# Optimization experiments

Measured on AMD Instinct MI355X. Metric: run time of the kernel, lower is better.

The kernel has to match this reference:

```python
import jax, jax.numpy as jnp
import numpy as np

HEADS = 8
DIM = 64      # dim
DH = 64       # dim_head
DK = 24       # dim_k (== dim_head_k * heads, required by reshape in forward)
DHK = 3       # dim_head_k (also conv groups)


def setup_inputs() -> dict:
    key = jax.random.key(0)
    ks = jax.random.split(key, 10)
    b, h, w = 4, 128, 128
    return {
        "x_in": jax.random.normal(ks[0], (b, h, w, DIM), jnp.float32),
        "illu_fea_trans": jax.random.normal(ks[1], (b, h, w, DIM), jnp.float32),
        "illu_map_trans": jax.random.normal(ks[2], (b, h, w, DK), jnp.float32),
        # Linear weights stored as [in, out] (torch stores [out, in]; math y = x @ W_in_out)
        "Wq": jax.random.normal(ks[3], (DIM, HEADS * DH), jnp.float32) * 0.05,
        "Wk": jax.random.normal(ks[4], (DK, HEADS * DHK), jnp.float32) * 0.05,
        "Wv": jax.random.normal(ks[5], (DIM, HEADS * DH), jnp.float32) * 0.05,
        "rescale": jnp.ones((HEADS, 1, 1), jnp.float32),
        "Wp": jax.random.normal(ks[6], (HEADS * DHK, DK), jnp.float32) * 0.05,
        "bp": jax.random.normal(ks[7], (DK,), jnp.float32) * 0.05,
        # grouped conv weights, OIHW: [out=24, in/groups=8, 3, 3]
        "conv1_w": jax.random.normal(ks[8], (DK, DK // DHK, 3, 3), jnp.float32) * 0.05,
        "conv2_w": jax.random.normal(ks[9], (DK, DK // DHK, 3, 3), jnp.float32) * 0.05,
    }


def _gconv(x_nchw, w_oihw):
    return jax.lax.conv_general_dilated(
        x_nchw, w_oihw, window_strides=(1, 1), padding='SAME',
        feature_group_count=DHK,
        dimension_numbers=('NCHW', 'OIHW', 'NCHW'))


def reference(x_in, illu_fea_trans, illu_map_trans, Wq, Wk, Wv, rescale, Wp, bp, conv1_w, conv2_w):
    b, h, w, c = x_in.shape
    n = h * w
    # projections
    q = (x_in.reshape(b, n, c) @ Wq).reshape(b, n, HEADS, DH)
    k_inp = illu_map_trans.reshape(b, n, DK) @ Wk            # [b, n, heads*dhk]
    v = (illu_fea_trans.reshape(b, n, c) @ Wv).reshape(b, n, HEADS, DH)
    kh = k_inp.reshape(b, n, HEADS, DHK)
    q = q / (DIM ** 0.5)  # note: scaled by sqrt(dim), not sqrt(dim_head)
    # channel-wise cross-attention: attn over channel dims, contracting tokens n
    attn = jnp.einsum('bnhk,bnhd->bhkd', kh, q) * rescale[None]  # [b, heads, dhk, dh]
    attn = jax.nn.softmax(attn, axis=-1)
    out = jnp.einsum('bhkd,bnhd->bnkh', attn, v)             # [b, n, dhk, heads]
    out = out.reshape(b, n, DHK * HEADS) @ Wp + bp           # proj
    out = out.reshape(b, h, w, DK)
    # positional branch: two grouped 3x3 convs with exact GELU on k_inp
    kx = k_inp.reshape(b, h, w, DK).transpose(0, 3, 1, 2)    # NCHW
    y = _gconv(kx, conv1_w)
    y = jax.nn.gelu(y, approximate=False)
    y = _gconv(y, conv2_w)
    return out + y.transpose(0, 2, 3, 1)
```

## Files before the change

kernel.cpp:

```cpp
#include <hip/hip_runtime.h>
#include <math.h>

#define HEADS 8
#define DIM   64
#define DK    24
#define DHK   3
#define BB    4
#define HH    128
#define WW    128
#define NN    (HH*WW)
#define QSCALE 0.125f

__global__ __launch_bounds__(1024) void s_reduce(
    const float* __restrict__ imap,
    const float* __restrict__ x,
    float* __restrict__ Sp_part,
    float* __restrict__ Pt)
{
    __shared__ float part[16 * 1540];
    const int tid = threadIdx.x;
    const int blk = blockIdx.x;
    const int b = blk >> 6, chunk = blk & 63;
    const int w = tid >> 6, lane = tid & 63;
    const int cq = lane & 15;
    const int ig = lane >> 4;

    const long tok0 = (long)b * NN + chunk * 256 + w * 16;
    const float* xp = x    + tok0 * 64 + cq * 4;
    const float* mp = imap + tok0 * 24 + ig * 6;

    float acc[6][4];
    #pragma unroll
    for (int r = 0; r < 6; ++r)
        #pragma unroll
        for (int q = 0; q < 4; ++q) acc[r][q] = 0.f;

    #pragma unroll 4
    for (int t = 0; t < 16; ++t) {
        float4 xv = *(const float4*)(xp + t * 64);
        float2 m0 = *(const float2*)(mp + t * 24);
        float2 m1 = *(const float2*)(mp + t * 24 + 2);
        float2 m2 = *(const float2*)(mp + t * 24 + 4);
        float mm[6] = {m0.x, m0.y, m1.x, m1.y, m2.x, m2.y};
        #pragma unroll
        for (int r = 0; r < 6; ++r) {
            acc[r][0] += mm[r] * xv.x;
            acc[r][1] += mm[r] * xv.y;
            acc[r][2] += mm[r] * xv.z;
            acc[r][3] += mm[r] * xv.w;
        }
    }

    float* pp = part + w * 1540;
    #pragma unroll
    for (int r = 0; r < 6; ++r) {
        float4 v = {acc[r][0], acc[r][1], acc[r][2], acc[r][3]};
        *(float4*)(pp + (ig * 6 + r) * 64 + cq * 4) = v;
    }
    __syncthreads();

    for (int e = tid; e < 1536; e += 1024) {
        float s = 0.f;
        #pragma unroll
        for (int ww = 0; ww < 16; ++ww) s += part[ww * 1540 + e];
        Sp_part[(long)blk * 1536 + e] = s;
    }
    if (blk < 4)
        for (int e = tid; e < 1536; e += 1024) Pt[blk * 1536 + e] = 0.f;
}

__global__ __launch_bounds__(256) void attn_fused(
    const float* __restrict__ Sp_part,
    const float* __restrict__ Wk,
    const float* __restrict__ Wq,
    const float* __restrict__ Wv,
    const float* __restrict__ rescale,
    const float* __restrict__ Wp,
    float* __restrict__ Pt)
{
    __shared__ float Sp_l[1536];
    __shared__ float sS[192];
    __shared__ float sP[192];
    __shared__ float Wv_l[64 * 65];

    const int tid = threadIdx.x, blk = blockIdx.x;
    const int b = blk >> 3, h = blk & 7;
    const int w = tid >> 6, lane = tid & 63;

    {
        float s[6] = {0.f, 0.f, 0.f, 0.f, 0.f, 0.f};
        const float* p = Sp_part + (long)(b * 64) * 1536 + tid;
        #pragma unroll 8
        for (int pb = 0; pb < 64; ++pb)
            #pragma unroll
            for (int k = 0; k < 6; ++k)
                s[k] += p[(long)pb * 1536 + k * 256];
        #pragma unroll
        for (int k = 0; k < 6; ++k) Sp_l[tid + k * 256] = s[k];
    }
    for (int e = tid; e < 4096; e += 256) {
        int c = e >> 6, d = e & 63;
        Wv_l[c * 65 + d] = Wv[c * 512 + h * 64 + d];
    }
    __syncthreads();

    if (w < 3) {
        const float* wk = Wk + (h * 3 + w);
        float s = 0.f;
        #pragma unroll
        for (int i = 0; i < 24; ++i) s += wk[i * 24] * Sp_l[i * 64 + lane];
        sS[w * 64 + lane] = s;
    }
    __syncthreads();

    if (w < 3) {
        const float* wq = Wq + h * 64 + lane;
        const float* sr = sS + w * 64;
        float a = 0.f;
        #pragma unroll 8
        for (int c = 0; c < 64; ++c) a += sr[c] * wq[c * 512];
        a *= QSCALE * rescale[h];
        float mx = a;
        #pragma unroll
        for (int off = 32; off >= 1; off >>= 1)
            mx = fmaxf(mx, __shfl_xor(mx, off, 64));
        float e = expf(a - mx);
        float sum = e;
        #pragma unroll
        for (int off = 32; off >= 1; off >>= 1)
            sum += __shfl_xor(sum, off, 64);
        sP[w * 64 + lane] = e / sum;
    }
    __syncthreads();

    if (w < 3) {
        const float* pr = sP + w * 64;
        const float* wv = Wv_l + lane * 65;
        float m = 0.f;
        #pragma unroll
        for (int d = 0; d < 64; ++d) m += pr[d] * wv[d];
        sS[w * 64 + lane] = m;
    }
    __syncthreads();

    for (int q = tid; q < 1536; q += 256) {
        int o = q >> 6, c = q & 63;
        float v = 0.f;
        #pragma unroll
        for (int k = 0; k < 3; ++k)
            v += sS[k * 64 + c] * Wp[(k * 8 + h) * 24 + o];
        atomicAdd(&Pt[b * 1536 + o * 64 + c], v);
    }
}

__global__ __launch_bounds__(192, 2) void conv_fused(
    const float* __restrict__ imap, const float* __restrict__ Wk,
    const float* __restrict__ c1w,  const float* __restrict__ fea,
    const float* __restrict__ c2w,  const float* __restrict__ Pt,
    const float* __restrict__ bp,   float* __restrict__ outp)
{
    __shared__ __align__(16) float kbuf[144 * 28];
    __shared__ __align__(16) float y1l[100 * 28];

    const int tid = threadIdx.x;
    const int blk = blockIdx.x;
    const int b = blk >> 8, ti = (blk >> 4) & 15, tj = blk & 15;
    const int i0 = ti * 8, j0 = tj * 8;
    const int o = tid % 24, jj = tid / 24;
    const int g = o >> 3;

    if (tid < 144) {
        const int pi = tid / 12, pj = tid % 12;
        const int gi = i0 + pi - 2, gj = j0 + pj - 2;
        float kv[24];
        #pragma unroll
        for (int j = 0; j < 24; ++j) kv[j] = 0.f;
        if (gi >= 0 && gi < HH && gj >= 0 && gj < WW) {
            const float4* m4 = (const float4*)(imap + (((long)b * HH + gi) * WW + gj) * 24);
            float m[24];
            #pragma unroll
            for (int i = 0; i < 6; ++i) {
                float4 v = m4[i];
                m[4*i+0]=v.x; m[4*i+1]=v.y; m[4*i+2]=v.z; m[4*i+3]=v.w;
            }
            for (int i = 0; i < 24; ++i) {
                float mi = m[i];
                #pragma unroll
                for (int j = 0; j < 24; ++j) kv[j] += mi * Wk[i * 24 + j];
            }
        }
        #pragma unroll
        for (int j = 0; j < 24; ++j) kbuf[tid * 28 + j] = kv[j];
    }
    __syncthreads();

    {
        float wr[8][9];
        {
            const float4* wp = (const float4*)(c1w + o * 72);
            #pragma unroll
            for (int t = 0; t < 18; ++t) ((float4*)wr)[t] = wp[t];
        }
        for (int task = tid; task < 240; task += 192) {
            const int r = task / 24;
            float wc[3][3][8];
            #pragma unroll
            for (int slot = 0; slot < 2; ++slot)
                #pragma unroll
                for (int di = 0; di < 3; ++di) {
                    const float* p = kbuf + ((r + di) * 12 + slot) * 28 + g * 8;
                    *(float4*)&wc[slot][di][0] = *(const float4*)(p);
                    *(float4*)&wc[slot][di][4] = *(const float4*)(p + 4);
                }
            #pragma unroll
            for (int c = 0; c < 10; ++c) {
                const int s2 = (c + 2) % 3;
                #pragma unroll
                for (int di = 0; di < 3; ++di) {
                    const float* p = kbuf + ((r + di) * 12 + (c + 2)) * 28 + g * 8;
                    *(float4*)&wc[s2][di][0] = *(const float4*)(p);
                    *(float4*)&wc[s2][di][4] = *(const float4*)(p + 4);
                }
                float s = 0.f;
                #pragma unroll
                for (int dj = 0; dj < 3; ++dj) {
                    const int sl = (c + dj) % 3;
                    #pragma unroll
                    for (int di = 0; di < 3; ++di)
                        #pragma unroll
                        for (int ic = 0; ic < 8; ++ic)
                            s += wc[sl][di][ic] * wr[ic][di * 3 + dj];
                }
                const int gi = i0 + r - 1, gj = j0 + c - 1;
                float val = 0.f;
                if (gi >= 0 && gi < HH && gj >= 0 && gj < WW)
                    val = 0.5f * s * (1.f + erff(s * 0.70710678f));
                y1l[(r * 10 + c) * 28 + o] = val;
            }
        }
    }
    __syncthreads();

    float wr[8][9];
    {
        const float4* wp = (const float4*)(c2w + o * 72);
        #pragma unroll
        for (int t = 0; t < 18; ++t) ((float4*)wr)[t] = wp[t];
    }

    float acc[8];
    {
        const float bo = bp[o];
        #pragma unroll
        for (int ii = 0; ii < 8; ++ii) acc[ii] = bo;
        const float* PtRow = Pt + b * 1536 + o * 64;
        const float* feaB = fea + (((long)(b * HH + i0)) * WW + (j0 + jj)) * 64;
        for (int cq = 0; cq < 16; ++cq) {
            float4 p = *(const float4*)(PtRow + cq * 4);
            #pragma unroll
            for (int ii = 0; ii < 8; ++ii) {
                float4 f = *(const float4*)(feaB + (long)ii * WW * 64 + cq * 4);
                acc[ii] += f.x * p.x + f.y * p.y + f.z * p.z + f.w * p.w;
            }
        }
    }

    float win[3][3][8];
    #define LROW(R, SLOT)                                                     \
    {                                                                         \
        const float* rp_ = y1l + ((R) * 10 + jj) * 28 + g * 8;                \
        *(float4*)&win[SLOT][0][0] = *(const float4*)(rp_);                   \
        *(float4*)&win[SLOT][0][4] = *(const float4*)(rp_ + 4);               \
        *(float4*)&win[SLOT][1][0] = *(const float4*)(rp_ + 28);              \
        *(float4*)&win[SLOT][1][4] = *(const float4*)(rp_ + 32);              \
        *(float4*)&win[SLOT][2][0] = *(const float4*)(rp_ + 56);              \
        *(float4*)&win[SLOT][2][4] = *(const float4*)(rp_ + 60);              \
    }

    LROW(0, 0)
    LROW(1, 1)
    #pragma unroll
    for (int ii = 0; ii < 8; ++ii) {
        LROW(ii + 2, (ii + 2) % 3)
        float s = 0.f;
        #pragma unroll
        for (int di = 0; di < 3; ++di) {
            const int slot = (ii + di) % 3;
            #pragma unroll
            for (int dj = 0; dj < 3; ++dj)
                #pragma unroll
                for (int ic = 0; ic < 8; ++ic)
                    s += win[slot][dj][ic] * wr[ic][di * 3 + dj];
        }
        outp[((long)((b * HH + i0 + ii) * WW + j0)) * 24 + tid] = acc[ii] + s;
    }
    #undef LROW
}

extern "C" void kernel_launch(void* const* d_in, const int* in_sizes, int n_in,
                              void* d_out, int out_size, void* d_ws, size_t ws_size,
                              hipStream_t stream) {
    const float* x_in    = (const float*)d_in[0];
    const float* fea     = (const float*)d_in[1];
    const float* imap    = (const float*)d_in[2];
    const float* Wq      = (const float*)d_in[3];
    const float* Wk      = (const float*)d_in[4];
    const float* Wv      = (const float*)d_in[5];
    const float* rescale = (const float*)d_in[6];
    const float* Wp      = (const float*)d_in[7];
    const float* bp      = (const float*)d_in[8];
    const float* c1w     = (const float*)d_in[9];
    const float* c2w     = (const float*)d_in[10];
    float* out = (float*)d_out;

    float* ws      = (float*)d_ws;
    float* Sp_part = ws;
    float* Pt      = ws + 393216;

    s_reduce<<<256, 1024, 0, stream>>>(imap, x_in, Sp_part, Pt);
    attn_fused<<<32, 256, 0, stream>>>(Sp_part, Wk, Wq, Wv, rescale, Wp, Pt);
    conv_fused<<<BB * 256, 192, 0, stream>>>(imap, Wk, c1w, fea, c2w, Pt, bp, out);
}
```

Measured before the change: 157.7 us.

## Fuse attention kernel into conv kernel with per-batch spin-wait flag

Removes the separate attn_fused launch by having the first eight blocks of each batch in the conv kernel compute the per-head attention projection and atomically accumulate into Pt, then bump a per-batch counter. All conv blocks run the conv1+GELU stage first and then spin until the counter reaches eight before using Pt, so the attention work overlaps with the convolution and one launch gap disappears. Shared memory is unified into one buffer and the occupancy hint rises from 2 to 4 blocks per CU. The spin-wait relies on the producer blocks being resident, which risks deadlock if scheduling order differs, and it adds some serialization on those few blocks.

```diff
diff --git a/kernel.cpp b/kernel.cpp
--- a/kernel.cpp
+++ b/kernel.cpp
@@ -15,7 +15,8 @@
     const float* __restrict__ imap,
     const float* __restrict__ x,
     float* __restrict__ Sp_part,
-    float* __restrict__ Pt)
+    float* __restrict__ Pt,
+    int* __restrict__ sync_)
 {
     __shared__ float part[16 * 1540];
     const int tid = threadIdx.x;
@@ -67,105 +68,107 @@
     }
     if (blk < 4)
         for (int e = tid; e < 1536; e += 1024) Pt[blk * 1536 + e] = 0.f;
+    if (blk == 4 && tid < 4) sync_[tid] = 0;
 }
 
-__global__ __launch_bounds__(256) void attn_fused(
-    const float* __restrict__ Sp_part,
-    const float* __restrict__ Wk,
-    const float* __restrict__ Wq,
-    const float* __restrict__ Wv,
-    const float* __restrict__ rescale,
-    const float* __restrict__ Wp,
-    float* __restrict__ Pt)
-{
-    __shared__ float Sp_l[1536];
-    __shared__ float sS[192];
-    __shared__ float sP[192];
-    __shared__ float Wv_l[64 * 65];
-
-    const int tid = threadIdx.x, blk = blockIdx.x;
-    const int b = blk >> 3, h = blk & 7;
-    const int w = tid >> 6, lane = tid & 63;
-
-    {
-        float s[6] = {0.f, 0.f, 0.f, 0.f, 0.f, 0.f};
-        const float* p = Sp_part + (long)(b * 64) * 1536 + tid;
-        #pragma unroll 8
-        for (int pb = 0; pb < 64; ++pb)
-            #pragma unroll
-            for (int k = 0; k < 6; ++k)
-                s[k] += p[(long)pb * 1536 + k * 256];
-        #pragma unroll
-        for (int k = 0; k < 6; ++k) Sp_l[tid + k * 256] = s[k];
-    }
-    for (int e = tid; e < 4096; e += 256) {
-        int c = e >> 6, d = e & 63;
-        Wv_l[c * 65 + d] = Wv[c * 512 + h * 64 + d];
-    }
-    __syncthreads();
-
-    if (w < 3) {
-        const float* wk = Wk + (h * 3 + w);
-        float s = 0.f;
-        #pragma unroll
-        for (int i = 0; i < 24; ++i) s += wk[i * 24] * Sp_l[i * 64 + lane];
-        sS[w * 64 + lane] = s;
-    }
-    __syncthreads();
-
-    if (w < 3) {
-        const float* wq = Wq + h * 64 + lane;
-        const float* sr = sS + w * 64;
-        float a = 0.f;
-        #pragma unroll 8
-        for (int c = 0; c < 64; ++c) a += sr[c] * wq[c * 512];
-        a *= QSCALE * rescale[h];
-        float mx = a;
-        #pragma unroll
-        for (int off = 32; off >= 1; off >>= 1)
-            mx = fmaxf(mx, __shfl_xor(mx, off, 64));
-        float e = expf(a - mx);
-        float sum = e;
-        #pragma unroll
-        for (int off = 32; off >= 1; off >>= 1)
-            sum += __shfl_xor(sum, off, 64);
-        sP[w * 64 + lane] = e / sum;
-    }
-    __syncthreads();
-
-    if (w < 3) {
-        const float* pr = sP + w * 64;
-        const float* wv = Wv_l + lane * 65;
-        float m = 0.f;
-        #pragma unroll
-        for (int d = 0; d < 64; ++d) m += pr[d] * wv[d];
-        sS[w * 64 + lane] = m;
-    }
-    __syncthreads();
-
-    for (int q = tid; q < 1536; q += 256) {
-        int o = q >> 6, c = q & 63;
-        float v = 0.f;
-        #pragma unroll
-        for (int k = 0; k < 3; ++k)
-            v += sS[k * 64 + c] * Wp[(k * 8 + h) * 24 + o];
-        atomicAdd(&Pt[b * 1536 + o * 64 + c], v);
-    }
-}
-
-__global__ __launch_bounds__(192, 2) void conv_fused(
+__global__ __launch_bounds__(192, 4) void conv_attn(
     const float* __restrict__ imap, const float* __restrict__ Wk,
     const float* __restrict__ c1w,  const float* __restrict__ fea,
-    const float* __restrict__ c2w,  const float* __restrict__ Pt,
-    const float* __restrict__ bp,   float* __restrict__ outp)
+    const float* __restrict__ c2w,  const float* __restrict__ bp,
+    const float* __restrict__ Wq,   const float* __restrict__ Wv,
+    const float* __restrict__ rescale, const float* __restrict__ Wp,
+    const float* __restrict__ Sp_part,
+    float* __restrict__ Pt,
+    int* __restrict__ done2,
+    float* __restrict__ outp)
 {
-    __shared__ __align__(16) float kbuf[144 * 28];
-    __shared__ __align__(16) float y1l[100 * 28];
+    __shared__ __align__(16) float smem[6832];
 
     const int tid = threadIdx.x;
     const int blk = blockIdx.x;
-    const int b = blk >> 8, ti = (blk >> 4) & 15, tj = blk & 15;
+    const int b = blk >> 8, chunk = blk & 255;
+    const int ti = chunk >> 4, tj = chunk & 15;
     const int i0 = ti * 8, j0 = tj * 8;
+
+    if (chunk < 8) {
+        const int h = chunk;
+        float* Sp_l = smem;
+        float* sS   = smem + 1536;
+        float* sP   = smem + 1760;
+        float* Wv_l = smem + 1984;
+        {
+            const float* p = Sp_part + (long)(b * 64) * 1536 + tid * 8;
+            float a2[8];
+            #pragma unroll
+            for (int q = 0; q < 8; ++q) a2[q] = 0.f;
+            #pragma unroll 8
+            for (int pb = 0; pb < 64; ++pb) {
+                float4 u = *(const float4*)(p + (long)pb * 1536);
+                float4 v = *(const float4*)(p + (long)pb * 1536 + 4);
+                a2[0] += u.x; a2[1] += u.y; a2[2] += u.z; a2[3] += u.w;
+                a2[4] += v.x; a2[5] += v.y; a2[6] += v.z; a2[7] += v.w;
+            }
+            #pragma unroll
+            for (int q = 0; q < 8; ++q) Sp_l[tid * 8 + q] = a2[q];
+        }
+        for (int e = tid; e < 4096; e += 192) {
+            int c = e >> 6, d = e & 63;
+            Wv_l[c * 65 + d] = Wv[c * 512 + h * 64 + d];
+        }
+        __syncthreads();
+
+        const int w3 = tid >> 6, lane = tid & 63;
+        {
+            const float* wk = Wk + (h * 3 + w3);
+            float s = 0.f;
+            #pragma unroll
+            for (int i = 0; i < 24; ++i) s += wk[i * 24] * Sp_l[i * 64 + lane];
+            sS[w3 * 64 + lane] = s;
+        }
+        __syncthreads();
+        {
+            const float* sr = sS + w3 * 64;
+            float a = 0.f;
+            #pragma unroll 8
+            for (int c = 0; c < 64; ++c) a += sr[c] * Wq[c * 512 + h * 64 + lane];
+            a *= QSCALE * rescale[h];
+            float mx = a;
+            #pragma unroll
+            for (int off = 32; off >= 1; off >>= 1)
+                mx = fmaxf(mx, __shfl_xor(mx, off, 64));
+            float e = expf(a - mx);
+            float sum = e;
+            #pragma unroll
+            for (int off = 32; off >= 1; off >>= 1)
+                sum += __shfl_xor(sum, off, 64);
+            sP[w3 * 64 + lane] = e / sum;
+        }
+        __syncthreads();
+        {
+            const float* pr = sP + w3 * 64;
+            const float* wv = Wv_l + lane * 65;
+            float m = 0.f;
+            #pragma unroll
+            for (int d = 0; d < 64; ++d) m += pr[d] * wv[d];
+            sS[w3 * 64 + lane] = m;
+        }
+        __syncthreads();
+        for (int q = tid; q < 1536; q += 192) {
+            int o = q >> 6, c = q & 63;
+            float v = 0.f;
+            #pragma unroll
+            for (int k = 0; k < 3; ++k)
+                v += sS[k * 64 + c] * Wp[(k * 8 + h) * 24 + o];
+            atomicAdd(&Pt[b * 1536 + o * 64 + c], v);
+        }
+        __threadfence();
+        __syncthreads();
+        if (tid == 0) atomicAdd(&done2[b], 1);
+        __syncthreads();
+    }
+
+    float* kbuf = smem;
+    float* y1l  = smem + 4032;
     const int o = tid % 24, jj = tid / 24;
     const int g = o >> 3;
 
@@ -240,6 +243,12 @@
         }
     }
     __syncthreads();
+
+    if (tid == 0)
+        while (__hip_atomic_load(&done2[b], __ATOMIC_RELAXED, __HIP_MEMORY_SCOPE_AGENT) < 8)
+            __builtin_amdgcn_s_sleep(2);
+    __syncthreads();
+    __threadfence();
 
     float wr[8][9];
     {
@@ -316,8 +325,10 @@
     float* ws      = (float*)d_ws;
     float* Sp_part = ws;
     float* Pt      = ws + 393216;
-
-    s_reduce<<<256, 1024, 0, stream>>>(imap, x_in, Sp_part, Pt);
-    attn_fused<<<32, 256, 0, stream>>>(Sp_part, Wk, Wq, Wv, rescale, Wp, Pt);
-    conv_fused<<<BB * 256, 192, 0, stream>>>(imap, Wk, c1w, fea, c2w, Pt, bp, out);
+    int*   sync_   = (int*)(ws + 399360);
+
+    s_reduce<<<256, 1024, 0, stream>>>(imap, x_in, Sp_part, Pt, sync_);
+    conv_attn<<<BB * 256, 192, 0, stream>>>(imap, Wk, c1w, fea, c2w, bp,
+                                            Wq, Wv, rescale, Wp,
+                                            Sp_part, Pt, sync_, out);
 }
```

New measurement: 315.4 us. +100.0%, slower.
